# Kernel tuning notes

Hardware: AMD Instinct MI355X
Metric: run time of the kernel (lower is better)

The kernel has to match this reference:

```python
import jax, jax.numpy as jnp
import numpy as np


def setup_inputs() -> dict:
    key = jax.random.key(0)
    k1, k2, k3, k4, k5 = jax.random.split(key, 5)
    B, D, U = 16384, 512, 512
    scale = 1.0 / np.sqrt(D + U)
    return {
        "inputs": jax.random.normal(k1, (B, D), dtype=jnp.float32),
        "h_prev": jax.random.normal(k2, (B, U), dtype=jnp.float32),
        "Wz": jax.random.normal(k3, (D + U, U), dtype=jnp.float32) * scale,
        "Wr": jax.random.normal(k4, (D + U, U), dtype=jnp.float32) * scale,
        "Wh": jax.random.normal(k5, (D + U, U), dtype=jnp.float32) * scale,
    }


def reference(inputs, h_prev, Wz, Wr, Wh):
    # x_h: [B, D+U]
    x_h = jnp.concatenate([inputs, h_prev], axis=-1)
    z = jax.nn.sigmoid(x_h @ Wz)                     # update gate [B, U]
    r = jax.nn.sigmoid(x_h @ Wr)                     # reset gate  [B, U]
    h_hat = jnp.tanh(jnp.concatenate([inputs, r * h_prev], axis=-1) @ Wh)
    new_h = z * h_prev + (1.0 - z) * h_hat
    return new_h
```

## Files before the change

kernel.cpp:

```cpp
#include <hip/hip_runtime.h>
#include <hip/hip_bf16.h>
#include <stdint.h>

typedef __attribute__((ext_vector_type(8))) short short8;
typedef __attribute__((ext_vector_type(4))) float f32x4;
typedef unsigned short u16;

#define AS1 __attribute__((address_space(1)))
#define AS3 __attribute__((address_space(3)))

__device__ __forceinline__ u16 f2b(float f) {
  union { float f; uint32_t u; } c; c.f = f;
  uint32_t u = c.u;
  return (u16)((u + 0x7fffu + ((u >> 16) & 1u)) >> 16);
}
__device__ __forceinline__ float b2f(u16 b) {
  union { uint32_t u; float f; } c; c.u = ((uint32_t)b) << 16;
  return c.f;
}

__global__ void cvt_bf16_kernel(const float* __restrict__ src,
                                u16* __restrict__ dst, int n4) {
  int i = blockIdx.x * blockDim.x + threadIdx.x;
  if (i >= n4) return;
  const float4 v = reinterpret_cast<const float4*>(src)[i];
  ushort4 o;
  o.x = f2b(v.x); o.y = f2b(v.y); o.z = f2b(v.z); o.w = f2b(v.w);
  reinterpret_cast<ushort4*>(dst)[i] = o;
}

__global__ void cvt_transpose_kernel(const float* __restrict__ w0,
                                     const float* __restrict__ w1,
                                     const float* __restrict__ w2,
                                     u16* __restrict__ d0,
                                     u16* __restrict__ d1,
                                     u16* __restrict__ d2,
                                     int K, int N) {
  const float* src = (blockIdx.y == 0) ? w0 : (blockIdx.y == 1 ? w1 : w2);
  u16* dst = (blockIdx.y == 0) ? d0 : (blockIdx.y == 1 ? d1 : d2);
  int idx = blockIdx.x * blockDim.x + threadIdx.x;
  if (idx >= K * N) return;
  int k = idx / N, n = idx - k * N;
  dst[(size_t)n * K + k] = f2b(src[idx]);
}


#define BAR() do { __builtin_amdgcn_s_barrier(); __builtin_amdgcn_sched_barrier(0); } while (0)
#define VMW(n) asm volatile("s_waitcnt vmcnt(" #n ")" ::: "memory")

template <int NBN, int EPI>
__global__ __launch_bounds__(256, 3) void gemm_kernel(
    const u16* __restrict__ a1,
    const u16* __restrict__ a2,
    const u16* __restrict__ wt,
    const float* __restrict__ hprev,
    const u16* __restrict__ zb_in,
    u16* __restrict__ o_z,
    u16* __restrict__ o_rh,
    float* __restrict__ o_f) {
  constexpr int NT = 32;
  constexpr int ATILE_E = 4096;
  constexpr int BUF_E = 8192;

  __shared__ u16 lds[3 * BUF_E];

  const int tid = threadIdx.x;
  const int lane = tid & 63;
  const int wid = tid >> 6;
  const int wm = wid >> 1;
  const int wn = wid & 1;

  const int cpx = (128 * NBN) >> 3;
  const int wg = ((int)blockIdx.x & 7) * cpx + ((int)blockIdx.x >> 3);
  const int bn = wg & (NBN - 1);
  const int bm = wg / NBN;

  const int srow = wid * 16 + (lane >> 2);
  const int scol = ((lane & 3) ^ ((lane >> 3) & 3)) << 4;
  const size_t aoff = (size_t)srow * 1024 + scol;
  const size_t boff = (size_t)srow * 2048 + scol;
  const size_t abase_g = (size_t)bm * 131072;
  const size_t bbase_g = (size_t)bn * 262144;

  auto STAGE = [&](int ktn, u16* buf) {
    const char* asn = (ktn < 16) ? ((const char*)a1 + abase_g + (size_t)ktn * 64)
                                 : ((const char*)a2 + abase_g + (size_t)(ktn - 16) * 64);
    const char* bsn = (const char*)wt + bbase_g + (size_t)ktn * 64;
    __builtin_amdgcn_global_load_lds((const AS1 void*)(asn + aoff),
                                     (AS3 void*)(buf + wid * 512), 16, 0, 0);
    __builtin_amdgcn_global_load_lds((const AS1 void*)(asn + 65536 + aoff),
                                     (AS3 void*)(buf + 2048 + wid * 512), 16, 0, 0);
    __builtin_amdgcn_global_load_lds((const AS1 void*)(bsn + boff),
                                     (AS3 void*)(buf + ATILE_E + wid * 512), 16, 0, 0);
    __builtin_amdgcn_global_load_lds((const AS1 void*)(bsn + 131072 + boff),
                                     (AS3 void*)(buf + ATILE_E + 2048 + wid * 512), 16, 0, 0);
  };

  const int rsel = lane & 15;
  const int kg = lane >> 4;
  const int rcol = (kg ^ ((rsel >> 1) & 3)) << 4;
  const int abyte = (wm * 64 + rsel) * 64 + rcol;
  const int bbyte = 8192 + (wn * 64 + rsel) * 64 + rcol;

  f32x4 acc[4][4] = {};

  STAGE(0, lds);
  STAGE(1, lds + BUF_E);
  VMW(4);
  BAR();

  int cb = 0;
  for (int kt = 0; kt < NT; ++kt) {
    u16* cur = lds + cb * BUF_E;
    const bool st = (kt + 2) < NT;
    if (st) {
      int nb = cb + 2; if (nb >= 3) nb -= 3;
      STAGE(kt + 2, lds + nb * BUF_E);
    }
    short8 bv[4];
#pragma unroll
    for (int nf = 0; nf < 4; ++nf)
      bv[nf] = *(const short8*)((const char*)cur + bbyte + nf * 1024);
    __builtin_amdgcn_s_setprio(1);
#pragma unroll
    for (int mf = 0; mf < 4; ++mf) {
      const short8 av = *(const short8*)((const char*)cur + abyte + mf * 1024);
#pragma unroll
      for (int nf = 0; nf < 4; ++nf)
        acc[mf][nf] = __builtin_amdgcn_mfma_f32_16x16x32_bf16(av, bv[nf], acc[mf][nf], 0, 0, 0);
    }
    __builtin_amdgcn_s_setprio(0);
    if (st) VMW(4); else VMW(0);
    BAR();
    ++cb; if (cb == 3) cb = 0;
  }

  const int row0 = bm * 128 + wm * 64 + kg * 4;
  const int col0 = bn * 128 + wn * 64 + rsel;
  if constexpr (EPI == 0) {
    if (bn < 4) {
#pragma unroll
      for (int mf = 0; mf < 4; ++mf)
#pragma unroll
        for (int nf = 0; nf < 4; ++nf)
#pragma unroll
          for (int q = 0; q < 4; ++q) {
            const int row = row0 + mf * 16 + q;
            const int col = col0 + nf * 16;
            const float zf = 1.f / (1.f + __expf(-acc[mf][nf][q]));
            o_z[(size_t)row * 512 + col] = f2b(zf);
          }
    } else {
#pragma unroll
      for (int mf = 0; mf < 4; ++mf)
#pragma unroll
        for (int nf = 0; nf < 4; ++nf)
#pragma unroll
          for (int q = 0; q < 4; ++q) {
            const int row = row0 + mf * 16 + q;
            const int col = col0 + nf * 16 - 512;
            const size_t idx = (size_t)row * 512 + col;
            const float rf = 1.f / (1.f + __expf(-acc[mf][nf][q]));
            o_rh[idx] = f2b(rf * hprev[idx]);
          }
    }
  } else {
#pragma unroll
    for (int mf = 0; mf < 4; ++mf)
#pragma unroll
      for (int nf = 0; nf < 4; ++nf)
#pragma unroll
        for (int q = 0; q < 4; ++q) {
          const int row = row0 + mf * 16 + q;
          const int col = col0 + nf * 16;
          const size_t idx = (size_t)row * 512 + col;
          const float s = acc[mf][nf][q];
          const float hh = 2.f / (1.f + __expf(-2.f * s)) - 1.f;
          const float z = b2f(zb_in[idx]);
          o_f[idx] = z * hprev[idx] + (1.f - z) * hh;
        }
  }
}

extern "C" void kernel_launch(void* const* d_in, const int* in_sizes, int n_in,
                              void* d_out, int out_size, void* d_ws, size_t ws_size,
                              hipStream_t stream) {
  const float* inputs = (const float*)d_in[0];
  const float* h_prev = (const float*)d_in[1];
  const float* Wz = (const float*)d_in[2];
  const float* Wr = (const float*)d_in[3];
  const float* Wh = (const float*)d_in[4];
  float* out = (float*)d_out;

  const int B = 16384, D = 512, U = 512, K = 1024;

  u16* xb = (u16*)d_ws;
  u16* hb = xb + (size_t)B * D;
  u16* wzt = hb + (size_t)B * U;
  u16* wrt = wzt + (size_t)K * U;
  u16* wht = wrt + (size_t)K * U;
  u16* zb = wht + (size_t)K * U;
  u16* rhb = zb + (size_t)B * U;

  const int n4 = (B * D) / 4;
  cvt_bf16_kernel<<<(n4 + 255) / 256, 256, 0, stream>>>(inputs, xb, n4);
  cvt_bf16_kernel<<<(n4 + 255) / 256, 256, 0, stream>>>(h_prev, hb, n4);
  dim3 tg((K * U + 255) / 256, 3);
  cvt_transpose_kernel<<<tg, 256, 0, stream>>>(Wz, Wr, Wh, wzt, wrt, wht, K, U);

  gemm_kernel<8, 0><<<dim3(1024), 256, 0, stream>>>(xb, hb, wzt, h_prev, nullptr, zb, rhb, nullptr);
  gemm_kernel<4, 1><<<dim3(512), 256, 0, stream>>>(xb, rhb, wht, h_prev, zb, nullptr, nullptr, out);
}
```

Before: 114.7 us.

## Rewrite GEMMs as 8-wave 256-row tiles with interleaved load/MFMA ping-pong schedule

Replaces the 256-thread, 128x128-tile triple-buffered GEMM with a 512-thread kernel. Tiles are 256x256 for the gate GEMM and 256x128 for the candidate GEMM, with K steps of 64, double-buffered LDS and a new XOR swizzle. The main loop interleaves partial LDS reads, global-to-LDS staging and MFMA quarter-blocks between explicit barriers, so loads overlap compute and each tile reuses operands more. In exchange it drops to one workgroup per CU, launches fewer blocks, and adds many barriers and register pressure.

```diff
diff --git a/kernel.cpp b/kernel.cpp
--- a/kernel.cpp
+++ b/kernel.cpp
@@ -45,11 +45,13 @@
 }
 
 
-#define BAR() do { __builtin_amdgcn_s_barrier(); __builtin_amdgcn_sched_barrier(0); } while (0)
-#define VMW(n) asm volatile("s_waitcnt vmcnt(" #n ")" ::: "memory")
-
-template <int NBN, int EPI>
-__global__ __launch_bounds__(256, 3) void gemm_kernel(
+#define BARO() do { __builtin_amdgcn_s_barrier(); __builtin_amdgcn_sched_barrier(0); } while (0)
+#define LGKM0() do { asm volatile("s_waitcnt lgkmcnt(0)" ::: "memory"); __builtin_amdgcn_sched_barrier(0); } while (0)
+#define VMW(n) do { asm volatile("s_waitcnt vmcnt(" #n ")" ::: "memory"); __builtin_amdgcn_sched_barrier(0); } while (0)
+#define PRIO_MM(MB, NB) do { __builtin_amdgcn_s_setprio(1); mm(MB, NB); __builtin_amdgcn_s_setprio(0); } while (0)
+
+template <int GATES>
+__global__ __launch_bounds__(512, 1) void gemm8_kernel(
     const u16* __restrict__ a1,
     const u16* __restrict__ a2,
     const u16* __restrict__ wt,
@@ -58,89 +60,123 @@
     u16* __restrict__ o_z,
     u16* __restrict__ o_rh,
     float* __restrict__ o_f) {
-  constexpr int NT = 32;
-  constexpr int ATILE_E = 4096;
-  constexpr int BUF_E = 8192;
-
-  __shared__ u16 lds[3 * BUF_E];
+  constexpr int NT = 16;
+  constexpr int NITER = 8;
+  constexpr int BN = GATES ? 256 : 128;
+  constexpr int MQ = GATES ? 4 : 2;
+  constexpr int AHALF = GATES ? 16384 : 8192;
+  constexpr int DBUF_E = GATES ? 32768 : 24576;
+  constexpr int DB1 = DBUF_E * 2;
+
+  __shared__ u16 lds[2 * DBUF_E];
+  const char* ldsb = (const char*)lds;
 
   const int tid = threadIdx.x;
   const int lane = tid & 63;
   const int wid = tid >> 6;
-  const int wm = wid >> 1;
-  const int wn = wid & 1;
-
-  const int cpx = (128 * NBN) >> 3;
-  const int wg = ((int)blockIdx.x & 7) * cpx + ((int)blockIdx.x >> 3);
-  const int bn = wg & (NBN - 1);
-  const int bm = wg / NBN;
-
-  const int srow = wid * 16 + (lane >> 2);
-  const int scol = ((lane & 3) ^ ((lane >> 3) & 3)) << 4;
-  const size_t aoff = (size_t)srow * 1024 + scol;
-  const size_t boff = (size_t)srow * 2048 + scol;
-  const size_t abase_g = (size_t)bm * 131072;
-  const size_t bbase_g = (size_t)bn * 262144;
-
-  auto STAGE = [&](int ktn, u16* buf) {
-    const char* asn = (ktn < 16) ? ((const char*)a1 + abase_g + (size_t)ktn * 64)
-                                 : ((const char*)a2 + abase_g + (size_t)(ktn - 16) * 64);
-    const char* bsn = (const char*)wt + bbase_g + (size_t)ktn * 64;
-    __builtin_amdgcn_global_load_lds((const AS1 void*)(asn + aoff),
-                                     (AS3 void*)(buf + wid * 512), 16, 0, 0);
-    __builtin_amdgcn_global_load_lds((const AS1 void*)(asn + 65536 + aoff),
-                                     (AS3 void*)(buf + 2048 + wid * 512), 16, 0, 0);
-    __builtin_amdgcn_global_load_lds((const AS1 void*)(bsn + boff),
-                                     (AS3 void*)(buf + ATILE_E + wid * 512), 16, 0, 0);
-    __builtin_amdgcn_global_load_lds((const AS1 void*)(bsn + 131072 + boff),
-                                     (AS3 void*)(buf + ATILE_E + 2048 + wid * 512), 16, 0, 0);
+  const int wm = GATES ? (wid >> 2) : (wid >> 1);
+  const int wn = GATES ? (wid & 3) : (wid & 1);
+
+  const int wg = ((int)blockIdx.x & 7) * 32 + ((int)blockIdx.x >> 3);
+  const int bn = wg & 3;
+  const int bm = wg >> 2;
+
+  const int srow8 = tid >> 3;
+  const int swzb = ((tid & 7) ^ (srow8 & 7)) << 4;
+  auto STAGE = [&](int t, int kind) {
+    if (t >= NT) return;
+    u16* dst = lds + (t & 1) * DBUF_E + kind * 8192 + wid * 512;
+    if (kind < 2) {
+      const char* src = ((t < 8) ? ((const char*)a1 + (size_t)t * 128)
+                                 : ((const char*)a2 + (size_t)(t - 8) * 128)) +
+                        (size_t)(bm * 256 + kind * 128 + srow8) * 1024 + swzb;
+      __builtin_amdgcn_global_load_lds((const AS1 void*)src, (AS3 void*)dst, 16, 0, 0);
+      __builtin_amdgcn_global_load_lds((const AS1 void*)(src + 65536), (AS3 void*)(dst + 4096), 16, 0, 0);
+    } else {
+      const char* src = (const char*)wt +
+                        (size_t)(bn * BN + (kind - 2) * 128 + srow8) * 2048 +
+                        (size_t)t * 128 + swzb;
+      __builtin_amdgcn_global_load_lds((const AS1 void*)src, (AS3 void*)dst, 16, 0, 0);
+      __builtin_amdgcn_global_load_lds((const AS1 void*)(src + 131072), (AS3 void*)(dst + 4096), 16, 0, 0);
+    }
   };
 
   const int rsel = lane & 15;
   const int kg = lane >> 4;
-  const int rcol = (kg ^ ((rsel >> 1) & 3)) << 4;
-  const int abyte = (wm * 64 + rsel) * 64 + rcol;
-  const int bbyte = 8192 + (wn * 64 + rsel) * 64 + rcol;
-
-  f32x4 acc[4][4] = {};
-
-  STAGE(0, lds);
-  STAGE(1, lds + BUF_E);
-  VMW(4);
-  BAR();
-
-  int cb = 0;
-  for (int kt = 0; kt < NT; ++kt) {
-    u16* cur = lds + cb * BUF_E;
-    const bool st = (kt + 2) < NT;
-    if (st) {
-      int nb = cb + 2; if (nb >= 3) nb -= 3;
-      STAGE(kt + 2, lds + nb * BUF_E);
-    }
-    short8 bv[4];
-#pragma unroll
-    for (int nf = 0; nf < 4; ++nf)
-      bv[nf] = *(const short8*)((const char*)cur + bbyte + nf * 1024);
-    __builtin_amdgcn_s_setprio(1);
-#pragma unroll
-    for (int mf = 0; mf < 4; ++mf) {
-      const short8 av = *(const short8*)((const char*)cur + abyte + mf * 1024);
-#pragma unroll
-      for (int nf = 0; nf < 4; ++nf)
-        acc[mf][nf] = __builtin_amdgcn_mfma_f32_16x16x32_bf16(av, bv[nf], acc[mf][nf], 0, 0, 0);
-    }
-    __builtin_amdgcn_s_setprio(0);
-    if (st) VMW(4); else VMW(0);
-    BAR();
-    ++cb; if (cb == 3) cb = 0;
+  const int sl0 = (kg ^ (rsel & 7)) << 4;
+  const int sl1 = ((4 + kg) ^ (rsel & 7)) << 4;
+  const int aoff0 = wm * AHALF + rsel * 128;
+  const int boff0 = 32768 + wn * 8192 + rsel * 128;
+
+  f32x4 acc[2 * MQ][4] = {};
+  short8 a[MQ][2], b[4][2];
+
+  auto ldA = [&](int DB, int mfb) {
+#pragma unroll
+    for (int mi = 0; mi < MQ; ++mi) {
+      a[mi][0] = *(const short8*)(ldsb + DB + aoff0 + (mfb + mi) * 2048 + sl0);
+      a[mi][1] = *(const short8*)(ldsb + DB + aoff0 + (mfb + mi) * 2048 + sl1);
+    }
+  };
+  auto ldB = [&](int DB, int nfb) {
+#pragma unroll
+    for (int ni = 0; ni < 2; ++ni) {
+      b[nfb + ni][0] = *(const short8*)(ldsb + DB + boff0 + (nfb + ni) * 2048 + sl0);
+      b[nfb + ni][1] = *(const short8*)(ldsb + DB + boff0 + (nfb + ni) * 2048 + sl1);
+    }
+  };
+  auto mm = [&](int mb, int nb) {
+#pragma unroll
+    for (int mi = 0; mi < MQ; ++mi)
+#pragma unroll
+      for (int ni = 0; ni < 2; ++ni) {
+        acc[mb + mi][nb + ni] = __builtin_amdgcn_mfma_f32_16x16x32_bf16(a[mi][0], b[nb + ni][0], acc[mb + mi][nb + ni], 0, 0, 0);
+        acc[mb + mi][nb + ni] = __builtin_amdgcn_mfma_f32_16x16x32_bf16(a[mi][1], b[nb + ni][1], acc[mb + mi][nb + ni], 0, 0, 0);
+      }
+  };
+
+  if constexpr (GATES) {
+    STAGE(0, 2); STAGE(0, 3); STAGE(0, 0); STAGE(0, 1); STAGE(1, 2); STAGE(1, 3);
+    VMW(4);
+  } else {
+    STAGE(0, 2); STAGE(0, 0); STAGE(0, 1); STAGE(1, 2);
+    VMW(2);
   }
-
-  const int row0 = bm * 128 + wm * 64 + kg * 4;
-  const int col0 = bn * 128 + wn * 64 + rsel;
-  if constexpr (EPI == 0) {
-    if (bn < 4) {
-#pragma unroll
-      for (int mf = 0; mf < 4; ++mf)
+  BARO();
+
+  for (int j = 0; j < NITER; ++j) {
+    const int t1 = 2 * j + 1, t2 = 2 * j + 2, t3 = 2 * j + 3;
+    ldA(0, 0); ldB(0, 0); STAGE(t1, 0);
+    BARO(); LGKM0(); PRIO_MM(0, 0); BARO();
+    ldB(0, 2); STAGE(t1, 1);
+    BARO(); LGKM0(); PRIO_MM(0, 2); BARO();
+    ldA(0, MQ); STAGE(t2, 2);
+    BARO(); LGKM0(); PRIO_MM(MQ, 2); BARO();
+    if constexpr (GATES) STAGE(t2, 3); else STAGE(t2, 0);
+    BARO(); PRIO_MM(MQ, 0);
+    if (j == NITER - 1) { VMW(0); } else { VMW(4); }
+    BARO();
+    ldA(DB1, 0); ldB(DB1, 0);
+    if constexpr (GATES) STAGE(t2, 0); else STAGE(t2, 1);
+    BARO(); LGKM0(); PRIO_MM(0, 0); BARO();
+    ldB(DB1, 2);
+    if constexpr (GATES) STAGE(t2, 1);
+    BARO(); LGKM0(); PRIO_MM(0, 2); BARO();
+    ldA(DB1, MQ); STAGE(t3, 2);
+    BARO(); LGKM0(); PRIO_MM(MQ, 2); BARO();
+    if constexpr (GATES) STAGE(t3, 3);
+    BARO(); PRIO_MM(MQ, 0);
+    if (j == NITER - 1) { VMW(0); }
+    else { if constexpr (GATES) VMW(4); else VMW(2); }
+    BARO();
+  }
+
+  const int row0 = bm * 256 + wm * (GATES ? 128 : 64) + kg * 4;
+  const int col0 = bn * BN + wn * 64 + rsel;
+  if constexpr (GATES) {
+    if (bn < 2) {
+#pragma unroll
+      for (int mf = 0; mf < 8; ++mf)
 #pragma unroll
         for (int nf = 0; nf < 4; ++nf)
 #pragma unroll
@@ -152,7 +188,7 @@
           }
     } else {
 #pragma unroll
-      for (int mf = 0; mf < 4; ++mf)
+      for (int mf = 0; mf < 8; ++mf)
 #pragma unroll
         for (int nf = 0; nf < 4; ++nf)
 #pragma unroll
@@ -208,6 +244,6 @@
   dim3 tg((K * U + 255) / 256, 3);
   cvt_transpose_kernel<<<tg, 256, 0, stream>>>(Wz, Wr, Wh, wzt, wrt, wht, K, U);
 
-  gemm_kernel<8, 0><<<dim3(1024), 256, 0, stream>>>(xb, hb, wzt, h_prev, nullptr, zb, rhb, nullptr);
-  gemm_kernel<4, 1><<<dim3(512), 256, 0, stream>>>(xb, rhb, wht, h_prev, zb, nullptr, nullptr, out);
-}
+  gemm8_kernel<1><<<dim3(256), 512, 0, stream>>>(xb, hb, wzt, h_prev, nullptr, zb, rhb, nullptr);
+  gemm8_kernel<0><<<dim3(256), 512, 0, stream>>>(xb, rhb, wht, h_prev, zb, nullptr, nullptr, out);
+}
```

After: 99.49 us. 13.2% less time.

## Restructure GEMM main loop to double-buffered BK=64 with split LDS reads

Applied to the files above, without the earlier changes.

Replaces the triple-buffered BK=32 GEMM loop with a double-buffered BK=64 pipeline. Each tile is split into four MFMA quadrants, interleaved with partial LDS register reads, next-tile staging, and finer waitcnt/barrier placement, with a new XOR swizzle for 128-byte rows. Occupancy hint drops from 3 to 2 blocks per CU. The epilogues now read h_prev from the bf16 copy instead of fp32, which cuts epilogue bandwidth but rounds h_prev in the final blend.

```diff
diff --git a/kernel.cpp b/kernel.cpp
--- a/kernel.cpp
+++ b/kernel.cpp
@@ -45,99 +45,128 @@
 }
 
 
-#define BAR() do { __builtin_amdgcn_s_barrier(); __builtin_amdgcn_sched_barrier(0); } while (0)
-#define VMW(n) asm volatile("s_waitcnt vmcnt(" #n ")" ::: "memory")
-
-template <int NBN, int EPI>
-__global__ __launch_bounds__(256, 3) void gemm_kernel(
+#define BAR() __builtin_amdgcn_s_barrier()
+#define SB() __builtin_amdgcn_sched_barrier(0)
+#define LG(n) do { asm volatile("s_waitcnt lgkmcnt(" #n ")" ::: "memory"); __builtin_amdgcn_sched_barrier(0); } while (0)
+#define VMW(n) do { asm volatile("s_waitcnt vmcnt(" #n ")" ::: "memory"); __builtin_amdgcn_sched_barrier(0); } while (0)
+
+template <int GATES>
+__global__ __launch_bounds__(256, 2) void gemm_rp_kernel(
     const u16* __restrict__ a1,
     const u16* __restrict__ a2,
     const u16* __restrict__ wt,
-    const float* __restrict__ hprev,
+    const u16* __restrict__ hb,
     const u16* __restrict__ zb_in,
     u16* __restrict__ o_z,
     u16* __restrict__ o_rh,
     float* __restrict__ o_f) {
-  constexpr int NT = 32;
-  constexpr int ATILE_E = 4096;
-  constexpr int BUF_E = 8192;
-
-  __shared__ u16 lds[3 * BUF_E];
+  constexpr int NT = 16;
+  constexpr int BUF_E = 16384;
+
+  __shared__ u16 lds[2 * BUF_E];
+  const char* ldsb = (const char*)lds;
 
   const int tid = threadIdx.x;
   const int lane = tid & 63;
   const int wid = tid >> 6;
-  const int wm = wid >> 1;
-  const int wn = wid & 1;
-
-  const int cpx = (128 * NBN) >> 3;
+  const int wm = wid >> 1, wn = wid & 1;
+
+  const int nbn = GATES ? 8 : 4;
+  const int cpx = GATES ? 128 : 64;
   const int wg = ((int)blockIdx.x & 7) * cpx + ((int)blockIdx.x >> 3);
-  const int bn = wg & (NBN - 1);
-  const int bm = wg / NBN;
-
-  const int srow = wid * 16 + (lane >> 2);
-  const int scol = ((lane & 3) ^ ((lane >> 3) & 3)) << 4;
-  const size_t aoff = (size_t)srow * 1024 + scol;
-  const size_t boff = (size_t)srow * 2048 + scol;
-  const size_t abase_g = (size_t)bm * 131072;
-  const size_t bbase_g = (size_t)bn * 262144;
-
-  auto STAGE = [&](int ktn, u16* buf) {
-    const char* asn = (ktn < 16) ? ((const char*)a1 + abase_g + (size_t)ktn * 64)
-                                 : ((const char*)a2 + abase_g + (size_t)(ktn - 16) * 64);
-    const char* bsn = (const char*)wt + bbase_g + (size_t)ktn * 64;
-    __builtin_amdgcn_global_load_lds((const AS1 void*)(asn + aoff),
-                                     (AS3 void*)(buf + wid * 512), 16, 0, 0);
-    __builtin_amdgcn_global_load_lds((const AS1 void*)(asn + 65536 + aoff),
-                                     (AS3 void*)(buf + 2048 + wid * 512), 16, 0, 0);
-    __builtin_amdgcn_global_load_lds((const AS1 void*)(bsn + boff),
-                                     (AS3 void*)(buf + ATILE_E + wid * 512), 16, 0, 0);
-    __builtin_amdgcn_global_load_lds((const AS1 void*)(bsn + 131072 + boff),
-                                     (AS3 void*)(buf + ATILE_E + 2048 + wid * 512), 16, 0, 0);
+  const int bn = wg & (nbn - 1);
+  const int bm = wg / nbn;
+
+  const int srow = tid >> 3;
+  const int swzb = ((tid & 7) ^ (srow & 7)) << 4;
+  auto STG_A = [&](int t, u16* buf) {
+    if (t >= NT) return;
+    const char* base = (t < 8) ? ((const char*)a1 + (size_t)t * 128)
+                               : ((const char*)a2 + (size_t)(t - 8) * 128);
+#pragma unroll
+    for (int i = 0; i < 4; ++i) {
+      const char* src = base + (size_t)(bm * 128 + i * 32 + srow) * 1024 + swzb;
+      __builtin_amdgcn_global_load_lds((const AS1 void*)src,
+                                       (AS3 void*)(buf + i * 2048 + wid * 512), 16, 0, 0);
+    }
+  };
+  auto STG_B = [&](int t, u16* buf) {
+    if (t >= NT) return;
+#pragma unroll
+    for (int i = 0; i < 4; ++i) {
+      const char* src = (const char*)wt +
+                        (size_t)(bn * 128 + i * 32 + srow) * 2048 +
+                        (size_t)t * 128 + swzb;
+      __builtin_amdgcn_global_load_lds((const AS1 void*)src,
+                                       (AS3 void*)(buf + 8192 + i * 2048 + wid * 512), 16, 0, 0);
+    }
   };
 
   const int rsel = lane & 15;
   const int kg = lane >> 4;
-  const int rcol = (kg ^ ((rsel >> 1) & 3)) << 4;
-  const int abyte = (wm * 64 + rsel) * 64 + rcol;
-  const int bbyte = 8192 + (wn * 64 + rsel) * 64 + rcol;
+  const int sl0 = (kg ^ (rsel & 7)) << 4;
+  const int sl1 = ((4 + kg) ^ (rsel & 7)) << 4;
+  const int aoff0 = (wm * 64 + rsel) * 128;
+  const int boff0 = 16384 + (wn * 64 + rsel) * 128;
 
   f32x4 acc[4][4] = {};
-
-  STAGE(0, lds);
-  STAGE(1, lds + BUF_E);
-  VMW(4);
-  BAR();
-
-  int cb = 0;
-  for (int kt = 0; kt < NT; ++kt) {
-    u16* cur = lds + cb * BUF_E;
-    const bool st = (kt + 2) < NT;
-    if (st) {
-      int nb = cb + 2; if (nb >= 3) nb -= 3;
-      STAGE(kt + 2, lds + nb * BUF_E);
-    }
-    short8 bv[4];
-#pragma unroll
-    for (int nf = 0; nf < 4; ++nf)
-      bv[nf] = *(const short8*)((const char*)cur + bbyte + nf * 1024);
+  short8 aLO[2][2], aHI[2][2];
+  short8 b01E[2][2], b01O[2][2];
+  short8 b23[2][2];
+
+  auto RD_A = [&](auto& dst, int bufB, int mfb) {
+#pragma unroll
+    for (int mi = 0; mi < 2; ++mi) {
+      dst[mi][0] = *(const short8*)(ldsb + bufB + aoff0 + (mfb + mi) * 2048 + sl0);
+      dst[mi][1] = *(const short8*)(ldsb + bufB + aoff0 + (mfb + mi) * 2048 + sl1);
+    }
+  };
+  auto RD_B = [&](auto& dst, int bufB, int nfb) {
+#pragma unroll
+    for (int ni = 0; ni < 2; ++ni) {
+      dst[ni][0] = *(const short8*)(ldsb + bufB + boff0 + (nfb + ni) * 2048 + sl0);
+      dst[ni][1] = *(const short8*)(ldsb + bufB + boff0 + (nfb + ni) * 2048 + sl1);
+    }
+  };
+  auto MM = [&](auto& A, auto& Bv, int mb, int nb) {
     __builtin_amdgcn_s_setprio(1);
 #pragma unroll
-    for (int mf = 0; mf < 4; ++mf) {
-      const short8 av = *(const short8*)((const char*)cur + abyte + mf * 1024);
-#pragma unroll
-      for (int nf = 0; nf < 4; ++nf)
-        acc[mf][nf] = __builtin_amdgcn_mfma_f32_16x16x32_bf16(av, bv[nf], acc[mf][nf], 0, 0, 0);
-    }
+    for (int ks = 0; ks < 2; ++ks)
+#pragma unroll
+      for (int mi = 0; mi < 2; ++mi)
+#pragma unroll
+        for (int ni = 0; ni < 2; ++ni)
+          acc[mb + mi][nb + ni] = __builtin_amdgcn_mfma_f32_16x16x32_bf16(
+              A[mi][ks], Bv[ni][ks], acc[mb + mi][nb + ni], 0, 0, 0);
     __builtin_amdgcn_s_setprio(0);
-    if (st) VMW(4); else VMW(0);
-    BAR();
-    ++cb; if (cb == 3) cb = 0;
+  };
+
+  auto TILE = [&](int t, int pB, int npB, auto& b01c, auto& b01n) {
+    u16* npbuf = lds + npB / 2;
+    RD_B(b23, pB, 2); STG_B(t + 1, npbuf); SB();
+    BAR(); LG(4); MM(aLO, b01c, 0, 0);
+    RD_A(aHI, pB, 2); STG_A(t + 1, npbuf); SB();
+    BAR(); LG(4); MM(aLO, b23, 0, 2);
+    BAR(); LG(0); MM(aHI, b23, 2, 2);
+    VMW(0); BAR();
+    if (t + 1 < NT) { RD_A(aLO, npB, 0); RD_B(b01n, npB, 0); }
+    SB();
+    MM(aHI, b01c, 2, 0);
+  };
+
+  STG_B(0, lds); STG_A(0, lds);
+  VMW(0); BAR();
+  RD_A(aLO, 0, 0); RD_B(b01E, 0, 0); SB();
+
+#pragma unroll 1
+  for (int j = 0; j < 8; ++j) {
+    TILE(2 * j, 0, 32768, b01E, b01O);
+    TILE(2 * j + 1, 32768, 0, b01O, b01E);
   }
 
   const int row0 = bm * 128 + wm * 64 + kg * 4;
   const int col0 = bn * 128 + wn * 64 + rsel;
-  if constexpr (EPI == 0) {
+  if constexpr (GATES) {
     if (bn < 4) {
 #pragma unroll
       for (int mf = 0; mf < 4; ++mf)
@@ -161,7 +190,7 @@
             const int col = col0 + nf * 16 - 512;
             const size_t idx = (size_t)row * 512 + col;
             const float rf = 1.f / (1.f + __expf(-acc[mf][nf][q]));
-            o_rh[idx] = f2b(rf * hprev[idx]);
+            o_rh[idx] = f2b(rf * b2f(hb[idx]));
           }
     }
   } else {
@@ -177,7 +206,7 @@
           const float s = acc[mf][nf][q];
           const float hh = 2.f / (1.f + __expf(-2.f * s)) - 1.f;
           const float z = b2f(zb_in[idx]);
-          o_f[idx] = z * hprev[idx] + (1.f - z) * hh;
+          o_f[idx] = z * b2f(hb[idx]) + (1.f - z) * hh;
         }
   }
 }
@@ -208,6 +237,6 @@
   dim3 tg((K * U + 255) / 256, 3);
   cvt_transpose_kernel<<<tg, 256, 0, stream>>>(Wz, Wr, Wh, wzt, wrt, wht, K, U);
 
-  gemm_kernel<8, 0><<<dim3(1024), 256, 0, stream>>>(xb, hb, wzt, h_prev, nullptr, zb, rhb, nullptr);
-  gemm_kernel<4, 1><<<dim3(512), 256, 0, stream>>>(xb, rhb, wht, h_prev, zb, nullptr, nullptr, out);
-}
+  gemm_rp_kernel<1><<<dim3(1024), 256, 0, stream>>>(xb, hb, wzt, hb, nullptr, zb, rhb, nullptr);
+  gemm_rp_kernel<0><<<dim3(512), 256, 0, stream>>>(xb, rhb, wht, hb, zb, nullptr, nullptr, out);
+}
```

New measurement: 101.5 us. 1.13x faster.

## Restructure GEMM main loop with BK=64, direct-to-register B loads, and split-phase pipelining

Applied to the files above, without the earlier changes.

The GEMM kernels are rewritten to use a K-tile of 64 with double-buffered LDS for A only. B fragments are now loaded from global memory straight into registers, ping-ponging between two register sets, and each tile is split into four MFMA quarters interleaved with staged loads, barriers and lgkm/vm waits. The epilogues now read h_prev as the bf16 copy instead of fp32, which halves those reads but adds rounding to the final blend. The aim is to raise MFMA overlap and cut LDS traffic. The cost is more register pressure (occupancy hint drops from 3 to 2) and uncoalesced global B loads.

```diff
diff --git a/kernel.cpp b/kernel.cpp
--- a/kernel.cpp
+++ b/kernel.cpp
@@ -45,126 +45,137 @@
 }
 
 
-#define BAR() do { __builtin_amdgcn_s_barrier(); __builtin_amdgcn_sched_barrier(0); } while (0)
-#define VMW(n) asm volatile("s_waitcnt vmcnt(" #n ")" ::: "memory")
-
-template <int NBN, int EPI>
-__global__ __launch_bounds__(256, 3) void gemm_kernel(
-    const u16* __restrict__ a1,
-    const u16* __restrict__ a2,
+#define BAR() __builtin_amdgcn_s_barrier()
+#define SB() __builtin_amdgcn_sched_barrier(0)
+#define LG(n) do { asm volatile("s_waitcnt lgkmcnt(" #n ")" ::: "memory"); __builtin_amdgcn_sched_barrier(0); } while (0)
+#define VMW(n) do { asm volatile("s_waitcnt vmcnt(" #n ")" ::: "memory"); __builtin_amdgcn_sched_barrier(0); } while (0)
+
+#define GEMM_PROLOG(NBN, CPX)                                              \
+  constexpr int NT = 16;                                                   \
+  __shared__ u16 lds[2 * 8192];                                            \
+  const char* ldsb = (const char*)lds;                                     \
+  const int tid = threadIdx.x, lane = tid & 63, wid = tid >> 6;            \
+  const int wm = wid >> 1, wn = wid & 1;                                   \
+  const int wg = ((int)blockIdx.x & 7) * (CPX) + ((int)blockIdx.x >> 3);   \
+  const int bn = wg & ((NBN) - 1), bm = wg / (NBN);                        \
+  const int srow = tid >> 3;                                               \
+  const int swzb = ((tid & 7) ^ (srow & 7)) << 4;                          \
+  const int rsel = lane & 15, kg = lane >> 4;                              \
+  const int sl0 = (kg ^ (rsel & 7)) << 4;                                  \
+  const int sl1 = ((4 + kg) ^ (rsel & 7)) << 4;                            \
+  const int aoff = (wm * 64 + rsel) * 128;                                 \
+  const char* wtl = (const char*)wt +                                      \
+      (size_t)(bn * 128 + wn * 64 + rsel) * 2048 + kg * 16;
+
+#define DEF_STG_A(SRC_LO, SRC_HI)                                          \
+  auto STG_A01 = [&](int t) {                                              \
+    if (t >= NT) return;                                                   \
+    char* dst = (char*)lds + (t & 1) * 16384 + wid * 1024;    \
+    const char* base = (t < 8) ? ((const char*)(SRC_LO) + (size_t)t * 128) \
+                               : ((const char*)(SRC_HI) + (size_t)(t - 8) * 128); \
+    _Pragma("unroll")                                                      \
+    for (int i = 0; i < 2; ++i) {                                          \
+      const char* s = base + (size_t)(bm * 128 + i * 32 + srow) * 1024 + swzb; \
+      __builtin_amdgcn_global_load_lds((const AS1 void*)s,                 \
+                                       (AS3 void*)(dst + i * 4096), 16, 0, 0); \
+    }                                                                      \
+  };                                                                       \
+  auto STG_A23 = [&](int t) {                                              \
+    if (t >= NT) return;                                                   \
+    char* dst = (char*)lds + (t & 1) * 16384 + wid * 1024;    \
+    const char* base = (t < 8) ? ((const char*)(SRC_LO) + (size_t)t * 128) \
+                               : ((const char*)(SRC_HI) + (size_t)(t - 8) * 128); \
+    _Pragma("unroll")                                                      \
+    for (int i = 2; i < 4; ++i) {                                          \
+      const char* s = base + (size_t)(bm * 128 + i * 32 + srow) * 1024 + swzb; \
+      __builtin_amdgcn_global_load_lds((const AS1 void*)s,                 \
+                                       (AS3 void*)(dst + i * 4096), 16, 0, 0); \
+    }                                                                      \
+  };
+
+#define DEF_HELPERS                                                        \
+  auto RD_ALO = [&](int t) {                                               \
+    const char* p = ldsb + (t & 1) * 16384 + aoff;                         \
+    _Pragma("unroll")                                                      \
+    for (int mi = 0; mi < 2; ++mi) {                                       \
+      aLO[mi][0] = *(const short8*)(p + mi * 2048 + sl0);                  \
+      aLO[mi][1] = *(const short8*)(p + mi * 2048 + sl1);                  \
+    }                                                                      \
+  };                                                                       \
+  auto RD_AHI = [&](int t) {                                               \
+    const char* p = ldsb + (t & 1) * 16384 + aoff;                         \
+    _Pragma("unroll")                                                      \
+    for (int mi = 0; mi < 2; ++mi) {                                       \
+      aHI[mi][0] = *(const short8*)(p + (2 + mi) * 2048 + sl0);            \
+      aHI[mi][1] = *(const short8*)(p + (2 + mi) * 2048 + sl1);            \
+    }                                                                      \
+  };                                                                       \
+  auto LDB01 = [&](auto& d, int t) {                                       \
+    if (t >= NT) return;                                                   \
+    const char* p = wtl + (size_t)t * 128;                                 \
+    _Pragma("unroll")                                                      \
+    for (int nf = 0; nf < 2; ++nf) {                                       \
+      d[nf][0] = *(const short8*)(p + nf * 32768);                         \
+      d[nf][1] = *(const short8*)(p + nf * 32768 + 64);                    \
+    }                                                                      \
+  };                                                                       \
+  auto LDB23 = [&](auto& d, int t) {                                       \
+    if (t >= NT) return;                                                   \
+    const char* p = wtl + (size_t)t * 128;                                 \
+    _Pragma("unroll")                                                      \
+    for (int nf = 2; nf < 4; ++nf) {                                       \
+      d[nf][0] = *(const short8*)(p + nf * 32768);                         \
+      d[nf][1] = *(const short8*)(p + nf * 32768 + 64);                    \
+    }                                                                      \
+  };                                                                       \
+  auto MM = [&](auto& A, auto& Bv, int mb, int nb) {                       \
+    __builtin_amdgcn_s_setprio(1);                                         \
+    _Pragma("unroll")                                                      \
+    for (int ks = 0; ks < 2; ++ks)                                         \
+      _Pragma("unroll")                                                    \
+      for (int mi = 0; mi < 2; ++mi)                                       \
+        _Pragma("unroll")                                                  \
+        for (int ni = 0; ni < 2; ++ni)                                     \
+          acc[mb + mi][nb + ni] = __builtin_amdgcn_mfma_f32_16x16x32_bf16( \
+              A[mi][ks], Bv[nb + ni][ks], acc[mb + mi][nb + ni], 0, 0, 0); \
+    __builtin_amdgcn_s_setprio(0);                                         \
+  };
+
+#define TILE(t, bc, bnx)                                                   \
+  do {                                                                     \
+    RD_AHI(t); LDB01(bnx, (t) + 1); STG_A01((t) + 1);                      \
+    BAR(); LG(4); MM(aLO, bc, 0, 0);                                       \
+    LDB23(bnx, (t) + 1); STG_A23((t) + 1);                                 \
+    BAR(); LG(0); MM(aLO, bc, 0, 2);                                       \
+    BAR(); MM(aHI, bc, 2, 2);                                              \
+    VMW(0); BAR();                                                         \
+    if ((t) + 1 < NT) RD_ALO((t) + 1);                                     \
+    SB(); MM(aHI, bc, 2, 0);                                               \
+  } while (0)
+
+__global__ __launch_bounds__(256, 2) void gates_k(
+    const u16* __restrict__ xb, const u16* __restrict__ hb,
     const u16* __restrict__ wt,
-    const float* __restrict__ hprev,
-    const u16* __restrict__ zb_in,
-    u16* __restrict__ o_z,
-    u16* __restrict__ o_rh,
-    float* __restrict__ o_f) {
-  constexpr int NT = 32;
-  constexpr int ATILE_E = 4096;
-  constexpr int BUF_E = 8192;
-
-  __shared__ u16 lds[3 * BUF_E];
-
-  const int tid = threadIdx.x;
-  const int lane = tid & 63;
-  const int wid = tid >> 6;
-  const int wm = wid >> 1;
-  const int wn = wid & 1;
-
-  const int cpx = (128 * NBN) >> 3;
-  const int wg = ((int)blockIdx.x & 7) * cpx + ((int)blockIdx.x >> 3);
-  const int bn = wg & (NBN - 1);
-  const int bm = wg / NBN;
-
-  const int srow = wid * 16 + (lane >> 2);
-  const int scol = ((lane & 3) ^ ((lane >> 3) & 3)) << 4;
-  const size_t aoff = (size_t)srow * 1024 + scol;
-  const size_t boff = (size_t)srow * 2048 + scol;
-  const size_t abase_g = (size_t)bm * 131072;
-  const size_t bbase_g = (size_t)bn * 262144;
-
-  auto STAGE = [&](int ktn, u16* buf) {
-    const char* asn = (ktn < 16) ? ((const char*)a1 + abase_g + (size_t)ktn * 64)
-                                 : ((const char*)a2 + abase_g + (size_t)(ktn - 16) * 64);
-    const char* bsn = (const char*)wt + bbase_g + (size_t)ktn * 64;
-    __builtin_amdgcn_global_load_lds((const AS1 void*)(asn + aoff),
-                                     (AS3 void*)(buf + wid * 512), 16, 0, 0);
-    __builtin_amdgcn_global_load_lds((const AS1 void*)(asn + 65536 + aoff),
-                                     (AS3 void*)(buf + 2048 + wid * 512), 16, 0, 0);
-    __builtin_amdgcn_global_load_lds((const AS1 void*)(bsn + boff),
-                                     (AS3 void*)(buf + ATILE_E + wid * 512), 16, 0, 0);
-    __builtin_amdgcn_global_load_lds((const AS1 void*)(bsn + 131072 + boff),
-                                     (AS3 void*)(buf + ATILE_E + 2048 + wid * 512), 16, 0, 0);
-  };
-
-  const int rsel = lane & 15;
-  const int kg = lane >> 4;
-  const int rcol = (kg ^ ((rsel >> 1) & 3)) << 4;
-  const int abyte = (wm * 64 + rsel) * 64 + rcol;
-  const int bbyte = 8192 + (wn * 64 + rsel) * 64 + rcol;
-
+    u16* __restrict__ o_z, u16* __restrict__ o_rh) {
+  GEMM_PROLOG(8, 128)
+  DEF_STG_A(xb, hb)
   f32x4 acc[4][4] = {};
-
-  STAGE(0, lds);
-  STAGE(1, lds + BUF_E);
-  VMW(4);
-  BAR();
-
-  int cb = 0;
-  for (int kt = 0; kt < NT; ++kt) {
-    u16* cur = lds + cb * BUF_E;
-    const bool st = (kt + 2) < NT;
-    if (st) {
-      int nb = cb + 2; if (nb >= 3) nb -= 3;
-      STAGE(kt + 2, lds + nb * BUF_E);
-    }
-    short8 bv[4];
-#pragma unroll
-    for (int nf = 0; nf < 4; ++nf)
-      bv[nf] = *(const short8*)((const char*)cur + bbyte + nf * 1024);
-    __builtin_amdgcn_s_setprio(1);
-#pragma unroll
-    for (int mf = 0; mf < 4; ++mf) {
-      const short8 av = *(const short8*)((const char*)cur + abyte + mf * 1024);
-#pragma unroll
-      for (int nf = 0; nf < 4; ++nf)
-        acc[mf][nf] = __builtin_amdgcn_mfma_f32_16x16x32_bf16(av, bv[nf], acc[mf][nf], 0, 0, 0);
-    }
-    __builtin_amdgcn_s_setprio(0);
-    if (st) VMW(4); else VMW(0);
-    BAR();
-    ++cb; if (cb == 3) cb = 0;
+  short8 aLO[2][2], aHI[2][2], bE[4][2], bO[4][2];
+  DEF_HELPERS
+
+  STG_A01(0); STG_A23(0); LDB01(bE, 0); LDB23(bE, 0);
+  VMW(0); BAR();
+  RD_ALO(0); SB();
+
+#pragma unroll 1
+  for (int j = 0; j < 8; ++j) {
+    TILE(2 * j, bE, bO);
+    TILE(2 * j + 1, bO, bE);
   }
 
   const int row0 = bm * 128 + wm * 64 + kg * 4;
   const int col0 = bn * 128 + wn * 64 + rsel;
-  if constexpr (EPI == 0) {
-    if (bn < 4) {
-#pragma unroll
-      for (int mf = 0; mf < 4; ++mf)
-#pragma unroll
-        for (int nf = 0; nf < 4; ++nf)
-#pragma unroll
-          for (int q = 0; q < 4; ++q) {
-            const int row = row0 + mf * 16 + q;
-            const int col = col0 + nf * 16;
-            const float zf = 1.f / (1.f + __expf(-acc[mf][nf][q]));
-            o_z[(size_t)row * 512 + col] = f2b(zf);
-          }
-    } else {
-#pragma unroll
-      for (int mf = 0; mf < 4; ++mf)
-#pragma unroll
-        for (int nf = 0; nf < 4; ++nf)
-#pragma unroll
-          for (int q = 0; q < 4; ++q) {
-            const int row = row0 + mf * 16 + q;
-            const int col = col0 + nf * 16 - 512;
-            const size_t idx = (size_t)row * 512 + col;
-            const float rf = 1.f / (1.f + __expf(-acc[mf][nf][q]));
-            o_rh[idx] = f2b(rf * hprev[idx]);
-          }
-    }
-  } else {
+  if (bn < 4) {
 #pragma unroll
     for (int mf = 0; mf < 4; ++mf)
 #pragma unroll
@@ -173,13 +184,61 @@
         for (int q = 0; q < 4; ++q) {
           const int row = row0 + mf * 16 + q;
           const int col = col0 + nf * 16;
+          const float zf = 1.f / (1.f + __expf(-acc[mf][nf][q]));
+          o_z[(size_t)row * 512 + col] = f2b(zf);
+        }
+  } else {
+#pragma unroll
+    for (int mf = 0; mf < 4; ++mf)
+#pragma unroll
+      for (int nf = 0; nf < 4; ++nf)
+#pragma unroll
+        for (int q = 0; q < 4; ++q) {
+          const int row = row0 + mf * 16 + q;
+          const int col = col0 + nf * 16 - 512;
           const size_t idx = (size_t)row * 512 + col;
-          const float s = acc[mf][nf][q];
-          const float hh = 2.f / (1.f + __expf(-2.f * s)) - 1.f;
-          const float z = b2f(zb_in[idx]);
-          o_f[idx] = z * hprev[idx] + (1.f - z) * hh;
+          const float rf = 1.f / (1.f + __expf(-acc[mf][nf][q]));
+          o_rh[idx] = f2b(rf * b2f(hb[idx]));
         }
   }
+}
+
+__global__ __launch_bounds__(256, 2) void cand_k(
+    const u16* __restrict__ xb, const u16* __restrict__ rhb,
+    const u16* __restrict__ wt, const u16* __restrict__ hb,
+    const u16* __restrict__ zb_in, float* __restrict__ o_f) {
+  GEMM_PROLOG(4, 64)
+  DEF_STG_A(xb, rhb)
+  f32x4 acc[4][4] = {};
+  short8 aLO[2][2], aHI[2][2], bE[4][2], bO[4][2];
+  DEF_HELPERS
+
+  STG_A01(0); STG_A23(0); LDB01(bE, 0); LDB23(bE, 0);
+  VMW(0); BAR();
+  RD_ALO(0); SB();
+
+#pragma unroll 1
+  for (int j = 0; j < 8; ++j) {
+    TILE(2 * j, bE, bO);
+    TILE(2 * j + 1, bO, bE);
+  }
+
+  const int row0 = bm * 128 + wm * 64 + kg * 4;
+  const int col0 = bn * 128 + wn * 64 + rsel;
+#pragma unroll
+  for (int mf = 0; mf < 4; ++mf)
+#pragma unroll
+    for (int nf = 0; nf < 4; ++nf)
+#pragma unroll
+      for (int q = 0; q < 4; ++q) {
+        const int row = row0 + mf * 16 + q;
+        const int col = col0 + nf * 16;
+        const size_t idx = (size_t)row * 512 + col;
+        const float s = acc[mf][nf][q];
+        const float hh = 2.f / (1.f + __expf(-2.f * s)) - 1.f;
+        const float z = b2f(zb_in[idx]);
+        o_f[idx] = z * b2f(hb[idx]) + (1.f - z) * hh;
+      }
 }
 
 extern "C" void kernel_launch(void* const* d_in, const int* in_sizes, int n_in,
@@ -208,6 +267,6 @@
   dim3 tg((K * U + 255) / 256, 3);
   cvt_transpose_kernel<<<tg, 256, 0, stream>>>(Wz, Wr, Wh, wzt, wrt, wht, K, U);
 
-  gemm_kernel<8, 0><<<dim3(1024), 256, 0, stream>>>(xb, hb, wzt, h_prev, nullptr, zb, rhb, nullptr);
-  gemm_kernel<4, 1><<<dim3(512), 256, 0, stream>>>(xb, rhb, wht, h_prev, zb, nullptr, nullptr, out);
-}
+  gates_k<<<dim3(1024), 256, 0, stream>>>(xb, hb, wzt, zb, rhb);
+  cand_k<<<dim3(512), 256, 0, stream>>>(xb, rhb, wht, hb, zb, out);
+}
```

Measured after the change: 151.4 us. 1.32x slower.
